# Performance work log

Measured on AMD Instinct MI355X. Metric: run time of the kernel, lower is better.

## Reference

```python
import jax, jax.numpy as jnp
import numpy as np
from jax import lax

NUM_COLS = 4
NUM_ROWS = 4
C = 16          # in_channels
K = 3           # kernel_size
B, H, Wd = 8, 128, 128
W_SCALE = 0.05  # keep activations stable through 16 chained ReLU convs


def setup_inputs() -> dict:
    key = jax.random.key(0)
    k1, k2 = jax.random.split(key, 2)
    x = jax.random.normal(k1, (B, C, H, Wd), dtype=jnp.float32)
    # one conv per grid cell: 3 input slots (left/below-prev/above), 3 output streams (right/up/down)
    W = jax.random.normal(k2, (NUM_COLS, NUM_ROWS, 3 * C, 3 * C, K, K), dtype=jnp.float32) * W_SCALE
    b = jnp.zeros((NUM_COLS, NUM_ROWS, 3 * C), dtype=jnp.float32)
    return {"input_tensor": x, "W": W, "b": b}


def _cell(w, bias, ins):
    # ins: list of 1..3 tensors [B, C, H, W]; zero-pad missing slots to 3*C channels
    if len(ins) < 3:
        pad_shape = (ins[0].shape[0], (3 - len(ins)) * C) + ins[0].shape[2:]
        ins = ins + [jnp.zeros(pad_shape, dtype=ins[0].dtype)]
    x = jnp.concatenate(ins, axis=1)  # [B, 3C, H, W]
    y = lax.conv_general_dilated(
        x, w, window_strides=(1, 1), padding="SAME",
        dimension_numbers=("NCHW", "OIHW", "NCHW"))
    y = jax.nn.relu(y + bias[None, :, None, None])
    right, up, down = jnp.split(y, 3, axis=1)  # each [B, C, H, W]
    return (right, up, down)


def reference(input_tensor, W, b):
    # Wavefront sweep: columns left->right, rows top->bottom.
    # outs[row] holds the (right, up, down) tuple of the most recently computed
    # cell in that row (previous column until overwritten this column).
    outs = [None] * NUM_ROWS
    for col in range(NUM_COLS):
        for row in range(NUM_ROWS):
            if col == 0:
                ins = [input_tensor] if row == 0 else [outs[row - 1][-1]]
            else:
                if row == 0:
                    ins = [outs[row][0], outs[row + 1][1]]
                elif row == NUM_ROWS - 1:
                    ins = [outs[row][0], outs[row - 1][-1]]
                else:
                    ins = [outs[row][0], outs[row + 1][1], outs[row - 1][-1]]
            outs[row] = _cell(W[col, row], b[col, row], ins)
    return outs[-1][0]
```

## Files before the change

### kernel.cpp

```cpp
#include <hip/hip_runtime.h>

#define HW    128
#define PW    130
#define NCELL 16
#define ABUF_PER_CELL 23040
#define ABUF_TOTAL (NCELL * ABUF_PER_CELL)
#define NSTREAMS 15
#define BORDER_PX 516
#define BORDER_TASKS (NSTREAMS * 8 * BORDER_PX * 2)
#define SLOT 5632

typedef _Float16 half8 __attribute__((ext_vector_type(8)));
typedef _Float16 half4 __attribute__((ext_vector_type(4)));
typedef float    f32x4 __attribute__((ext_vector_type(4)));

#define GLD_LDS(gp, lp) __builtin_amdgcn_global_load_lds( \
    (const __attribute__((address_space(1))) void*)(gp),  \
    (__attribute__((address_space(3))) void*)(lp), 16, 0, 0)

__global__ void prep_w_border_k(const float* __restrict__ W,
                                _Float16* __restrict__ Abuf,
                                _Float16* __restrict__ sbase) {
    int idx = blockIdx.x * 256 + threadIdx.x;
    if (idx < ABUF_TOTAL) {
        int j = idx & 7;
        int t = idx >> 3;
        int co = t % 48;   t /= 48;
        int quad = t & 3;  t >>= 2;
        int chunk = t % 5; t /= 5;
        int slot = t % 3;  t /= 3;
        int cell = t;
        int g = chunk * 4 + quad;
        float v = 0.f;
        if (g < 18) {
            int kh = g / 6, r6 = g % 6;
            int kw = r6 >> 1, cg = r6 & 1;
            int ci = slot * 16 + cg * 8 + j;
            v = W[((size_t)(cell * 48 + co) * 48 + ci) * 9 + kh * 3 + kw];
        }
        Abuf[idx] = (_Float16)v;
        return;
    }
    int t = idx - ABUF_TOTAL;
    if (t >= BORDER_TASKS) return;
    int h  = t & 1;
    int pb = t >> 1;
    int p  = pb % BORDER_PX;
    int bb = pb / BORDER_PX;
    int y, x;
    if (p < 260) {
        y = (p < 130) ? 0 : (PW - 1);
        x = p - ((p < 130) ? 0 : 130);
    } else {
        int e = p - 260;
        y = 1 + (e >> 1);
        x = (e & 1) ? (PW - 1) : 0;
    }
    half8 z = {};
    *(half8*)(sbase + (size_t)bb * (PW * PW * 16)
              + ((size_t)y * PW + x) * 16 + h * 8) = z;
}

struct CellIO {
    const _Float16* in0; const _Float16* in1; const _Float16* in2;
    const _Float16* Ac; const float* bc;
    _Float16* o0; _Float16* o1; _Float16* o2;
    float* fout;
};

template<int LIVE, int NIN, bool FIN, bool XIN>
__device__ __forceinline__ void cell_body(const CellIO& P, int b, _Float16* xh,
                                          const float* xsrc)
{
    const int tid = threadIdx.x;
    const int bx = blockIdx.x, by = blockIdx.y;
    const int x0 = bx * 16, y0 = by * 16;
    const int lane = tid & 63, wv = tid >> 6;
    const int n = lane & 15, quad = lane >> 4;
    const int py0 = wv * 4;

    float bv[3][4];
    half8 a0[3][3];

    if constexpr (XIN) {
        for (int task = tid; task < 288; task += 256) {
            int ci = task / 18, iy = task - (task / 18) * 18;
            float v[18];
#pragma unroll
            for (int ix = 0; ix < 18; ++ix) v[ix] = 0.f;
            int gy = y0 + iy - 1;
            if ((unsigned)gy < (unsigned)HW) {
                const float* rp = xsrc + (((size_t)b * 16 + ci) * HW + gy) * HW + x0;
                f32x4 q0 = *(const f32x4*)(rp);
                f32x4 q1 = *(const f32x4*)(rp + 4);
                f32x4 q2 = *(const f32x4*)(rp + 8);
                f32x4 q3 = *(const f32x4*)(rp + 12);
#pragma unroll
                for (int j = 0; j < 4; ++j) {
                    v[1 + j] = q0[j]; v[5 + j] = q1[j];
                    v[9 + j] = q2[j]; v[13 + j] = q3[j];
                }
                if (x0 > 0)       v[0]  = rp[-1];
                if (x0 < HW - 16) v[17] = rp[16];
            }
            int cg = ci >> 3, cj = ci & 7;
#pragma unroll
            for (int ix = 0; ix < 18; ++ix)
                xh[(((iy * 2 + cg) * 18) + ix) * 8 + cj] = (_Float16)v[ix];
        }
        __syncthreads();
    } else {
        const _Float16* const ins[3] = {P.in0, P.in1, P.in2};
        auto stage = [&](int s) {
            const _Float16* src = ins[s] + (size_t)b * (PW * PW * 16)
                                 + ((size_t)(by * 16) * PW + bx * 16) * 16;
            _Float16* base = xh + s * SLOT;
#pragma unroll
            for (int k = 0; k < 3; ++k) {
                int kk = wv + k * 4;
                if (kk < 11) {
                    int u = kk * 64 + lane;
                    int iy = u / 36, r36 = u - iy * 36;
                    int cg = r36 / 18, ix = r36 - cg * 18;
                    GLD_LDS(src + (iy * PW + ix) * 16 + cg * 8, base + kk * 512);
                }
            }
        };
#pragma unroll
        for (int cot = 0; cot < 3; ++cot) {
            if (!(LIVE & (1 << cot))) continue;
#pragma unroll
            for (int r = 0; r < 4; ++r) bv[cot][r] = P.bc[cot * 16 + quad * 4 + r];
        }
        {
            const _Float16* As0 = P.Ac + quad * 384 + n * 8;
#pragma unroll
            for (int c = 0; c < 3; ++c)
#pragma unroll
                for (int cot = 0; cot < 3; ++cot) {
                    if (!(LIVE & (1 << cot))) continue;
                    a0[c][cot] = *(const half8*)(As0 + c * 1536 + cot * 128);
                }
        }
        asm volatile("" ::: "memory");
        stage(0);
        if constexpr (NIN >= 2) {
            asm volatile("" ::: "memory");
#pragma unroll
            for (int s = 1; s < NIN; ++s) stage(s);
            if (wv == 3) asm volatile("s_waitcnt vmcnt(%0)" :: "n"((NIN - 1) * 2) : "memory");
            else         asm volatile("s_waitcnt vmcnt(%0)" :: "n"((NIN - 1) * 3) : "memory");
            __builtin_amdgcn_s_barrier();
            asm volatile("" ::: "memory");
        } else {
            __syncthreads();
        }
    }

    int base_c[5];
#pragma unroll
    for (int c = 0; c < 5; ++c) {
        int g = c * 4 + quad;
        if (g >= 18) g = 0;
        int kh = g / 6, r6 = g % 6;
        int kw = r6 >> 1, cg = r6 & 1;
        base_c[c] = ((py0 + kh) * 2 + cg) * 18 + n + kw;
    }

    constexpr bool PIPE = (!XIN) && (NIN >= 2);
    f32x4 acc[3][4];
#pragma unroll
    for (int cot = 0; cot < 3; ++cot) {
        if (!(LIVE & (1 << cot))) continue;
#pragma unroll
        for (int r = 0; r < 4; ++r) {
            float bvv = XIN ? P.bc[cot * 16 + quad * 4 + r] : bv[cot][r];
#pragma unroll
            for (int nt = 0; nt < 4; ++nt) acc[cot][nt][r] = bvv;
        }
    }

    constexpr int NC = NIN * 5;
#pragma unroll
    for (int i = 0; i < NC; ++i) {
        int s, c;
        if constexpr (PIPE) {
            if (i < 3)                        { s = 0; c = i; }
            else if (i < 3 + 5 * (NIN - 1))   { s = 1 + (i - 3) / 5; c = (i - 3) % 5; }
            else                              { s = 0; c = i - 5 * (NIN - 1); }
        } else { s = i / 5; c = i % 5; }
        if (PIPE && i == 3) __syncthreads();

        const _Float16* sxh = xh + s * SLOT;
        half8 Bh[4];
#pragma unroll
        for (int nt = 0; nt < 4; ++nt)
            Bh[nt] = *(const half8*)(sxh + (base_c[c] + nt * 36) * 8);
        const _Float16* Ab = P.Ac + (size_t)(s * 5 + c) * 1536 + quad * 384 + n * 8;
        half8 ah[3];
#pragma unroll
        for (int cot = 0; cot < 3; ++cot) {
            if (!(LIVE & (1 << cot))) continue;
            if (!XIN && s == 0 && c < 3) ah[cot] = a0[c][cot];
            else                         ah[cot] = *(const half8*)(Ab + cot * 128);
        }
        __builtin_amdgcn_s_setprio(1);
#pragma unroll
        for (int cot = 0; cot < 3; ++cot) {
            if (!(LIVE & (1 << cot))) continue;
#pragma unroll
            for (int nt = 0; nt < 4; ++nt)
                acc[cot][nt] = __builtin_amdgcn_mfma_f32_16x16x32_f16(ah[cot], Bh[nt], acc[cot][nt], 0, 0, 0);
        }
        __builtin_amdgcn_s_setprio(0);
    }

    if constexpr (FIN) {
#pragma unroll
        for (int nt = 0; nt < 4; ++nt) {
            int y = y0 + py0 + nt, xg = x0 + n;
#pragma unroll
            for (int r = 0; r < 4; ++r) {
                float vv = acc[0][nt][r];
                P.fout[(((size_t)b * 16 + quad * 4 + r) * HW + y) * HW + xg] = vv > 0.f ? vv : 0.f;
            }
        }
    } else {
        _Float16* const outs[3] = {P.o0, P.o1, P.o2};
#pragma unroll
        for (int cot = 0; cot < 3; ++cot) {
            if (!(LIVE & (1 << cot))) continue;
            _Float16* op = outs[cot] + (size_t)b * (PW * PW * 16);
#pragma unroll
            for (int nt = 0; nt < 4; ++nt) {
                int y = y0 + py0 + nt;
                half4 hv;
#pragma unroll
                for (int r = 0; r < 4; ++r) {
                    float vv = acc[cot][nt][r];
                    hv[r] = (_Float16)(vv > 0.f ? vv : 0.f);
                }
                *(half4*)(op + ((size_t)(y + 1) * PW + x0 + n + 1) * 16 + quad * 4) = hv;
            }
        }
    }
}

template<int L0, int N0, int L1, int N1, bool FIN, bool XIN>
__global__ __launch_bounds__(256, 4) void cell_k(CellIO P0, CellIO P1,
                                                 const float* xsrc) {
    constexpr int MAXN = (N0 > N1) ? N0 : N1;
    __shared__ __align__(16) _Float16 xh[MAXN * SLOT];
    int b = blockIdx.z & 7;
    if constexpr (L1 > 0) {
        if (blockIdx.z >= 8) { cell_body<L1, N1, false, false>(P1, b, xh, nullptr); return; }
    }
    cell_body<L0, N0, FIN, XIN>(P0, b, xh, xsrc);
}

extern "C" void kernel_launch(void* const* d_in, const int* in_sizes, int n_in,
                              void* d_out, int out_size, void* d_ws, size_t ws_size,
                              hipStream_t stream) {
    const float* x  = (const float*)d_in[0];
    const float* W  = (const float*)d_in[1];
    const float* bi = (const float*)d_in[2];
    float* out = (float*)d_out;

    _Float16* Abuf = (_Float16*)d_ws;
    const size_t abytes = (size_t)NCELL * ABUF_PER_CELL * 2;
    _Float16* q = (_Float16*)((char*)d_ws + abytes);
    _Float16* sbase = q;
    const size_t S = (size_t)8 * PW * PW * 16;

    _Float16 *R[2][4], *U[4], *D[2][2];
    for (int pa = 0; pa < 2; ++pa)
        for (int r = 0; r < 4; ++r) { R[pa][r] = q; q += S; }
    U[0] = nullptr;
    for (int r = 1; r < 4; ++r) { U[r] = q; q += S; }
    D[0][0] = q; q += S; D[0][1] = q; q += S;
    D[1][0] = q; q += S; D[1][1] = q; q += S;

    hipLaunchKernelGGL(prep_w_border_k,
                       dim3((ABUF_TOTAL + BORDER_TASKS + 255) / 256),
                       dim3(256), 0, stream, W, Abuf, sbase);

    auto mkio = [&](int c, int r) -> CellIO {
        CellIO io{};
        if (c == 0) {
            io.in0 = (r == 0) ? nullptr : D[0][(r - 1) & 1];
        } else {
            io.in0 = R[(c - 1) & 1][r];
            if (r == 0)      io.in1 = U[1];
            else if (r == 3) io.in1 = D[c & 1][0];
            else { io.in1 = U[r + 1]; io.in2 = D[c & 1][(r - 1) & 1]; }
        }
        if (c < 3) {
            io.o0 = R[c & 1][r];
            if (r > 0) io.o1 = U[r];
            if (r < 3) io.o2 = D[c & 1][r & 1];
        } else {
            if (r < 3) io.o2 = D[1][r & 1];
            else       io.fout = out;
        }
        io.Ac = Abuf + (size_t)(c * 4 + r) * ABUF_PER_CELL;
        io.bc = bi + (size_t)(c * 4 + r) * 48;
        return io;
    };

    dim3 blk(256), g1(8, 8, 8), g2(8, 8, 16);
#define ONEX(c, r)       do { CellIO a = mkio(c, r); \
    hipLaunchKernelGGL((cell_k<5, 1, 0, 0, false, true>), g1, blk, 0, stream, a, a, x); } while (0)
#define ONE(L, N, c, r)  do { CellIO a = mkio(c, r); \
    hipLaunchKernelGGL((cell_k<L, N, 0, 0, false, false>), g1, blk, 0, stream, a, a, x); } while (0)
#define ONEF(c, r)       do { CellIO a = mkio(c, r); \
    hipLaunchKernelGGL((cell_k<1, 2, 0, 0, true, false>), g1, blk, 0, stream, a, a, x); } while (0)
#define TWO(L0, N0, c0, r0, L1, N1, c1, r1) do { \
    CellIO a = mkio(c0, r0), bb2 = mkio(c1, r1); \
    hipLaunchKernelGGL((cell_k<L0, N0, L1, N1, false, false>), g2, blk, 0, stream, a, bb2, x); } while (0)

    ONEX(0, 0);
    ONE(7, 1, 0, 1);
    TWO(7, 1, 0, 2,  5, 2, 1, 0);
    TWO(3, 1, 0, 3,  7, 3, 1, 1);
    TWO(7, 3, 1, 2,  5, 2, 2, 0);
    TWO(3, 2, 1, 3,  7, 3, 2, 1);
    TWO(7, 3, 2, 2,  4, 2, 3, 0);
    TWO(3, 2, 2, 3,  4, 3, 3, 1);
    ONE(4, 3, 3, 2);
    ONEF(3, 3);
#undef ONEX
#undef ONE
#undef ONEF
#undef TWO
}
```

Baseline: 165.1 us.

## Refine staged-input pipeline with finer vmcnt waits and split B-fragment loads

Shrinks the preloaded slot-0 weight fragments from three chunks to two and restarts the pipelined schedule after two chunks. The single __syncthreads is replaced by per-wave s_waitcnt vmcnt plus s_barrier at chunk boundaries, with a second wait before the third input slot, so later slots can still be in flight while earlier ones are consumed. B fragments are loaded in two halves interleaved with MFMAs to lower register pressure and overlap LDS reads with compute. The manual vmcnt counts depend on the exact number of outstanding global-to-LDS loads per wave, so any mismatch would cause a race.

```diff
diff --git a/kernel.cpp b/kernel.cpp
--- a/kernel.cpp
+++ b/kernel.cpp
@@ -80,7 +80,7 @@
     const int py0 = wv * 4;
 
     float bv[3][4];
-    half8 a0[3][3];
+    half8 a0[2][3];
 
     if constexpr (XIN) {
         for (int task = tid; task < 288; task += 256) {
@@ -135,7 +135,7 @@
         {
             const _Float16* As0 = P.Ac + quad * 384 + n * 8;
 #pragma unroll
-            for (int c = 0; c < 3; ++c)
+            for (int c = 0; c < 2; ++c)
 #pragma unroll
                 for (int cot = 0; cot < 3; ++cot) {
                     if (!(LIVE & (1 << cot))) continue;
@@ -185,34 +185,57 @@
     for (int i = 0; i < NC; ++i) {
         int s, c;
         if constexpr (PIPE) {
-            if (i < 3)                        { s = 0; c = i; }
-            else if (i < 3 + 5 * (NIN - 1))   { s = 1 + (i - 3) / 5; c = (i - 3) % 5; }
+            if (i < 2)                        { s = 0; c = i; }
+            else if (i < 2 + 5 * (NIN - 1))   { s = 1 + (i - 2) / 5; c = (i - 2) % 5; }
             else                              { s = 0; c = i - 5 * (NIN - 1); }
         } else { s = i / 5; c = i % 5; }
-        if (PIPE && i == 3) __syncthreads();
+
+        if constexpr (PIPE) {
+            if (i == 2) {
+                if constexpr (NIN == 3) {
+                    if (wv == 3) asm volatile("s_waitcnt vmcnt(2)" ::: "memory");
+                    else         asm volatile("s_waitcnt vmcnt(3)" ::: "memory");
+                } else {
+                    asm volatile("s_waitcnt vmcnt(0)" ::: "memory");
+                }
+                __builtin_amdgcn_s_barrier();
+                asm volatile("" ::: "memory");
+            }
+            if constexpr (NIN == 3) {
+                if (i == 7) {
+                    asm volatile("s_waitcnt vmcnt(0)" ::: "memory");
+                    __builtin_amdgcn_s_barrier();
+                    asm volatile("" ::: "memory");
+                }
+            }
+        }
 
         const _Float16* sxh = xh + s * SLOT;
-        half8 Bh[4];
-#pragma unroll
-        for (int nt = 0; nt < 4; ++nt)
-            Bh[nt] = *(const half8*)(sxh + (base_c[c] + nt * 36) * 8);
         const _Float16* Ab = P.Ac + (size_t)(s * 5 + c) * 1536 + quad * 384 + n * 8;
         half8 ah[3];
 #pragma unroll
         for (int cot = 0; cot < 3; ++cot) {
             if (!(LIVE & (1 << cot))) continue;
-            if (!XIN && s == 0 && c < 3) ah[cot] = a0[c][cot];
+            if (!XIN && s == 0 && c < 2) ah[cot] = a0[c][cot];
             else                         ah[cot] = *(const half8*)(Ab + cot * 128);
         }
-        __builtin_amdgcn_s_setprio(1);
-#pragma unroll
-        for (int cot = 0; cot < 3; ++cot) {
-            if (!(LIVE & (1 << cot))) continue;
-#pragma unroll
-            for (int nt = 0; nt < 4; ++nt)
-                acc[cot][nt] = __builtin_amdgcn_mfma_f32_16x16x32_f16(ah[cot], Bh[nt], acc[cot][nt], 0, 0, 0);
-        }
-        __builtin_amdgcn_s_setprio(0);
+#pragma unroll
+        for (int np = 0; np < 2; ++np) {
+            half8 Bh[2];
+#pragma unroll
+            for (int t = 0; t < 2; ++t)
+                Bh[t] = *(const half8*)(sxh + (base_c[c] + (np * 2 + t) * 36) * 8);
+            __builtin_amdgcn_s_setprio(1);
+#pragma unroll
+            for (int cot = 0; cot < 3; ++cot) {
+                if (!(LIVE & (1 << cot))) continue;
+#pragma unroll
+                for (int t = 0; t < 2; ++t)
+                    acc[cot][np * 2 + t] = __builtin_amdgcn_mfma_f32_16x16x32_f16(
+                        ah[cot], Bh[t], acc[cot][np * 2 + t], 0, 0, 0);
+            }
+            __builtin_amdgcn_s_setprio(0);
+        }
     }
 
     if constexpr (FIN) {
```

Measured after the change: 169.4 us. +2.6%, slower.

## Fold weight prep and border zeroing into the first cell kernel

Applied to the files above, without the earlier changes.

Removes the separate prep kernel that converted weights to fp16 MFMA layout and zeroed padded borders. The first cell kernel now builds its own cell-0 weights directly into LDS, and its 512 blocks share the remaining weight conversion for cells 1-15 plus the border zeroing. This saves one kernel launch and its serial dependency, at the cost of more LDS and extra work in the first cell kernel, which could lengthen it.

```diff
diff --git a/kernel.cpp b/kernel.cpp
--- a/kernel.cpp
+++ b/kernel.cpp
@@ -9,6 +9,10 @@
 #define BORDER_PX 516
 #define BORDER_TASKS (NSTREAMS * 8 * BORDER_PX * 2)
 #define SLOT 5632
+#define XA_HALFS 7680
+#define PREP_TASKS (15 * ABUF_PER_CELL)
+#define HEAD_TOT (PREP_TASKS + BORDER_TASKS)
+#define HEAD_SPAN ((HEAD_TOT + 511) / 512)
 
 typedef _Float16 half8 __attribute__((ext_vector_type(8)));
 typedef _Float16 half4 __attribute__((ext_vector_type(4)));
@@ -17,49 +21,6 @@
 #define GLD_LDS(gp, lp) __builtin_amdgcn_global_load_lds( \
     (const __attribute__((address_space(1))) void*)(gp),  \
     (__attribute__((address_space(3))) void*)(lp), 16, 0, 0)
-
-__global__ void prep_w_border_k(const float* __restrict__ W,
-                                _Float16* __restrict__ Abuf,
-                                _Float16* __restrict__ sbase) {
-    int idx = blockIdx.x * 256 + threadIdx.x;
-    if (idx < ABUF_TOTAL) {
-        int j = idx & 7;
-        int t = idx >> 3;
-        int co = t % 48;   t /= 48;
-        int quad = t & 3;  t >>= 2;
-        int chunk = t % 5; t /= 5;
-        int slot = t % 3;  t /= 3;
-        int cell = t;
-        int g = chunk * 4 + quad;
-        float v = 0.f;
-        if (g < 18) {
-            int kh = g / 6, r6 = g % 6;
-            int kw = r6 >> 1, cg = r6 & 1;
-            int ci = slot * 16 + cg * 8 + j;
-            v = W[((size_t)(cell * 48 + co) * 48 + ci) * 9 + kh * 3 + kw];
-        }
-        Abuf[idx] = (_Float16)v;
-        return;
-    }
-    int t = idx - ABUF_TOTAL;
-    if (t >= BORDER_TASKS) return;
-    int h  = t & 1;
-    int pb = t >> 1;
-    int p  = pb % BORDER_PX;
-    int bb = pb / BORDER_PX;
-    int y, x;
-    if (p < 260) {
-        y = (p < 130) ? 0 : (PW - 1);
-        x = p - ((p < 130) ? 0 : 130);
-    } else {
-        int e = p - 260;
-        y = 1 + (e >> 1);
-        x = (e & 1) ? (PW - 1) : 0;
-    }
-    half8 z = {};
-    *(half8*)(sbase + (size_t)bb * (PW * PW * 16)
-              + ((size_t)y * PW + x) * 16 + h * 8) = z;
-}
 
 struct CellIO {
     const _Float16* in0; const _Float16* in1; const _Float16* in2;
@@ -70,7 +31,9 @@
 
 template<int LIVE, int NIN, bool FIN, bool XIN>
 __device__ __forceinline__ void cell_body(const CellIO& P, int b, _Float16* xh,
-                                          const float* xsrc)
+                                          _Float16* xa, const float* xsrc,
+                                          const float* Wsrc, _Float16* abufg,
+                                          _Float16* sbaseg)
 {
     const int tid = threadIdx.x;
     const int bx = blockIdx.x, by = blockIdx.y;
@@ -108,6 +71,67 @@
             for (int ix = 0; ix < 18; ++ix)
                 xh[(((iy * 2 + cg) * 18) + ix) * 8 + cj] = (_Float16)v[ix];
         }
+        for (int a = tid; a < XA_HALFS; a += 256) {
+            int j = a & 7;
+            int t = a >> 3;
+            int co = t % 48;  t /= 48;
+            int qd = t & 3;   t >>= 2;
+            int ch = t;
+            int g = ch * 4 + qd;
+            float v = 0.f;
+            if (g < 18) {
+                int kh = g / 6, r6 = g % 6;
+                int kw = r6 >> 1, cg = r6 & 1;
+                int ci = cg * 8 + j;
+                v = Wsrc[((size_t)co * 48 + ci) * 9 + kh * 3 + kw];
+            }
+            xa[a] = (_Float16)v;
+        }
+        {
+            int blin = (blockIdx.z << 6) + (by << 3) + bx;
+            int i0 = blin * HEAD_SPAN;
+            int iend = i0 + HEAD_SPAN;
+            if (iend > HEAD_TOT) iend = HEAD_TOT;
+            for (int idx = i0 + tid; idx < iend; idx += 256) {
+                if (idx < PREP_TASKS) {
+                    int ii = idx + ABUF_PER_CELL;
+                    int j = ii & 7;
+                    int t = ii >> 3;
+                    int co = t % 48;   t /= 48;
+                    int qd = t & 3;    t >>= 2;
+                    int chunk = t % 5; t /= 5;
+                    int slot = t % 3;  t /= 3;
+                    int cell = t;
+                    int g = chunk * 4 + qd;
+                    float v = 0.f;
+                    if (g < 18) {
+                        int kh = g / 6, r6 = g % 6;
+                        int kw = r6 >> 1, cg = r6 & 1;
+                        int ci = slot * 16 + cg * 8 + j;
+                        v = Wsrc[((size_t)(cell * 48 + co) * 48 + ci) * 9 + kh * 3 + kw];
+                    }
+                    abufg[ii] = (_Float16)v;
+                } else {
+                    int t2 = idx - PREP_TASKS;
+                    int h  = t2 & 1;
+                    int pb = t2 >> 1;
+                    int p  = pb % BORDER_PX;
+                    int bb = pb / BORDER_PX;
+                    int y, x;
+                    if (p < 260) {
+                        y = (p < 130) ? 0 : (PW - 1);
+                        x = p - ((p < 130) ? 0 : 130);
+                    } else {
+                        int e = p - 260;
+                        y = 1 + (e >> 1);
+                        x = (e & 1) ? (PW - 1) : 0;
+                    }
+                    half8 z = {};
+                    *(half8*)(sbaseg + (size_t)bb * (PW * PW * 16)
+                              + ((size_t)y * PW + x) * 16 + h * 8) = z;
+                }
+            }
+        }
         __syncthreads();
     } else {
         const _Float16* const ins[3] = {P.in0, P.in1, P.in2};
@@ -196,13 +220,21 @@
 #pragma unroll
         for (int nt = 0; nt < 4; ++nt)
             Bh[nt] = *(const half8*)(sxh + (base_c[c] + nt * 36) * 8);
-        const _Float16* Ab = P.Ac + (size_t)(s * 5 + c) * 1536 + quad * 384 + n * 8;
         half8 ah[3];
-#pragma unroll
-        for (int cot = 0; cot < 3; ++cot) {
-            if (!(LIVE & (1 << cot))) continue;
-            if (!XIN && s == 0 && c < 3) ah[cot] = a0[c][cot];
-            else                         ah[cot] = *(const half8*)(Ab + cot * 128);
+        if constexpr (XIN) {
+#pragma unroll
+            for (int cot = 0; cot < 3; ++cot) {
+                if (!(LIVE & (1 << cot))) continue;
+                ah[cot] = *(const half8*)(xa + c * 1536 + quad * 384 + cot * 128 + n * 8);
+            }
+        } else {
+            const _Float16* Ab = P.Ac + (size_t)(s * 5 + c) * 1536 + quad * 384 + n * 8;
+#pragma unroll
+            for (int cot = 0; cot < 3; ++cot) {
+                if (!(LIVE & (1 << cot))) continue;
+                if (s == 0 && c < 3) ah[cot] = a0[c][cot];
+                else                 ah[cot] = *(const half8*)(Ab + cot * 128);
+            }
         }
         __builtin_amdgcn_s_setprio(1);
 #pragma unroll
@@ -248,14 +280,23 @@
 
 template<int L0, int N0, int L1, int N1, bool FIN, bool XIN>
 __global__ __launch_bounds__(256, 4) void cell_k(CellIO P0, CellIO P1,
-                                                 const float* xsrc) {
+                                                 const float* xsrc,
+                                                 const float* Wsrc,
+                                                 _Float16* abufg,
+                                                 _Float16* sbaseg) {
     constexpr int MAXN = (N0 > N1) ? N0 : N1;
-    __shared__ __align__(16) _Float16 xh[MAXN * SLOT];
+    constexpr int XAH = XIN ? XA_HALFS : 0;
+    __shared__ __align__(16) _Float16 xh[MAXN * SLOT + XAH];
     int b = blockIdx.z & 7;
     if constexpr (L1 > 0) {
-        if (blockIdx.z >= 8) { cell_body<L1, N1, false, false>(P1, b, xh, nullptr); return; }
-    }
-    cell_body<L0, N0, FIN, XIN>(P0, b, xh, xsrc);
+        if (blockIdx.z >= 8) {
+            cell_body<L1, N1, false, false>(P1, b, xh, nullptr, nullptr,
+                                            nullptr, nullptr, nullptr);
+            return;
+        }
+    }
+    cell_body<L0, N0, FIN, XIN>(P0, b, xh, XIN ? (xh + MAXN * SLOT) : nullptr,
+                                xsrc, Wsrc, abufg, sbaseg);
 }
 
 extern "C" void kernel_launch(void* const* d_in, const int* in_sizes, int n_in,
@@ -279,10 +320,6 @@
     for (int r = 1; r < 4; ++r) { U[r] = q; q += S; }
     D[0][0] = q; q += S; D[0][1] = q; q += S;
     D[1][0] = q; q += S; D[1][1] = q; q += S;
-
-    hipLaunchKernelGGL(prep_w_border_k,
-                       dim3((ABUF_TOTAL + BORDER_TASKS + 255) / 256),
-                       dim3(256), 0, stream, W, Abuf, sbase);
 
     auto mkio = [&](int c, int r) -> CellIO {
         CellIO io{};
@@ -309,14 +346,14 @@
 
     dim3 blk(256), g1(8, 8, 8), g2(8, 8, 16);
 #define ONEX(c, r)       do { CellIO a = mkio(c, r); \
-    hipLaunchKernelGGL((cell_k<5, 1, 0, 0, false, true>), g1, blk, 0, stream, a, a, x); } while (0)
+    hipLaunchKernelGGL((cell_k<5, 1, 0, 0, false, true>), g1, blk, 0, stream, a, a, x, W, Abuf, sbase); } while (0)
 #define ONE(L, N, c, r)  do { CellIO a = mkio(c, r); \
-    hipLaunchKernelGGL((cell_k<L, N, 0, 0, false, false>), g1, blk, 0, stream, a, a, x); } while (0)
+    hipLaunchKernelGGL((cell_k<L, N, 0, 0, false, false>), g1, blk, 0, stream, a, a, x, W, Abuf, sbase); } while (0)
 #define ONEF(c, r)       do { CellIO a = mkio(c, r); \
-    hipLaunchKernelGGL((cell_k<1, 2, 0, 0, true, false>), g1, blk, 0, stream, a, a, x); } while (0)
+    hipLaunchKernelGGL((cell_k<1, 2, 0, 0, true, false>), g1, blk, 0, stream, a, a, x, W, Abuf, sbase); } while (0)
 #define TWO(L0, N0, c0, r0, L1, N1, c1, r1) do { \
     CellIO a = mkio(c0, r0), bb2 = mkio(c1, r1); \
-    hipLaunchKernelGGL((cell_k<L0, N0, L1, N1, false, false>), g2, blk, 0, stream, a, bb2, x); } while (0)
+    hipLaunchKernelGGL((cell_k<L0, N0, L1, N1, false, false>), g2, blk, 0, stream, a, bb2, x, W, Abuf, sbase); } while (0)
 
     ONEX(0, 0);
     ONE(7, 1, 0, 1);
```

Measured after the change: 169.9 us. 2.9% more time.

## Read conv input tiles directly from global memory instead of staging in LDS

Applied to the files above, without the earlier changes.

Removes the global_load_lds staging of input halo tiles into shared memory and the barriers that go with it. Each lane now loads its MFMA B operands straight from the padded global activation buffers, relying on L1/L2 caching for reuse across the 3x3 taps. This cuts LDS use and synchronisation, which may allow more resident blocks, but adds redundant global loads and exposes global latency inside the MFMA loop.

```diff
diff --git a/kernel.cpp b/kernel.cpp
--- a/kernel.cpp
+++ b/kernel.cpp
@@ -8,15 +8,10 @@
 #define NSTREAMS 15
 #define BORDER_PX 516
 #define BORDER_TASKS (NSTREAMS * 8 * BORDER_PX * 2)
-#define SLOT 5632
 
 typedef _Float16 half8 __attribute__((ext_vector_type(8)));
 typedef _Float16 half4 __attribute__((ext_vector_type(4)));
 typedef float    f32x4 __attribute__((ext_vector_type(4)));
-
-#define GLD_LDS(gp, lp) __builtin_amdgcn_global_load_lds( \
-    (const __attribute__((address_space(1))) void*)(gp),  \
-    (__attribute__((address_space(3))) void*)(lp), 16, 0, 0)
 
 __global__ void prep_w_border_k(const float* __restrict__ W,
                                 _Float16* __restrict__ Abuf,
@@ -81,6 +76,7 @@
 
     float bv[3][4];
     half8 a0[3][3];
+    const _Float16* srcs[3];
 
     if constexpr (XIN) {
         for (int task = tid; task < 288; task += 256) {
@@ -111,21 +107,10 @@
         __syncthreads();
     } else {
         const _Float16* const ins[3] = {P.in0, P.in1, P.in2};
-        auto stage = [&](int s) {
-            const _Float16* src = ins[s] + (size_t)b * (PW * PW * 16)
-                                 + ((size_t)(by * 16) * PW + bx * 16) * 16;
-            _Float16* base = xh + s * SLOT;
-#pragma unroll
-            for (int k = 0; k < 3; ++k) {
-                int kk = wv + k * 4;
-                if (kk < 11) {
-                    int u = kk * 64 + lane;
-                    int iy = u / 36, r36 = u - iy * 36;
-                    int cg = r36 / 18, ix = r36 - cg * 18;
-                    GLD_LDS(src + (iy * PW + ix) * 16 + cg * 8, base + kk * 512);
-                }
-            }
-        };
+#pragma unroll
+        for (int s = 0; s < NIN; ++s)
+            srcs[s] = ins[s] + (size_t)b * (PW * PW * 16)
+                      + ((size_t)(by * 16) * PW + bx * 16) * 16;
 #pragma unroll
         for (int cot = 0; cot < 3; ++cot) {
             if (!(LIVE & (1 << cot))) continue;
@@ -142,29 +127,17 @@
                     a0[c][cot] = *(const half8*)(As0 + c * 1536 + cot * 128);
                 }
         }
-        asm volatile("" ::: "memory");
-        stage(0);
-        if constexpr (NIN >= 2) {
-            asm volatile("" ::: "memory");
-#pragma unroll
-            for (int s = 1; s < NIN; ++s) stage(s);
-            if (wv == 3) asm volatile("s_waitcnt vmcnt(%0)" :: "n"((NIN - 1) * 2) : "memory");
-            else         asm volatile("s_waitcnt vmcnt(%0)" :: "n"((NIN - 1) * 3) : "memory");
-            __builtin_amdgcn_s_barrier();
-            asm volatile("" ::: "memory");
-        } else {
-            __syncthreads();
-        }
-    }
-
-    int base_c[5];
+    }
+
+    int boff_c[5];
 #pragma unroll
     for (int c = 0; c < 5; ++c) {
         int g = c * 4 + quad;
         if (g >= 18) g = 0;
         int kh = g / 6, r6 = g % 6;
         int kw = r6 >> 1, cg = r6 & 1;
-        base_c[c] = ((py0 + kh) * 2 + cg) * 18 + n + kw;
+        if constexpr (XIN) boff_c[c] = ((py0 + kh) * 2 + cg) * 18 + n + kw;
+        else               boff_c[c] = ((py0 + kh) * PW + n + kw) * 16 + cg * 8;
     }
 
     constexpr bool PIPE = (!XIN) && (NIN >= 2);
@@ -189,13 +162,17 @@
             else if (i < 3 + 5 * (NIN - 1))   { s = 1 + (i - 3) / 5; c = (i - 3) % 5; }
             else                              { s = 0; c = i - 5 * (NIN - 1); }
         } else { s = i / 5; c = i % 5; }
-        if (PIPE && i == 3) __syncthreads();
-
-        const _Float16* sxh = xh + s * SLOT;
+
         half8 Bh[4];
-#pragma unroll
-        for (int nt = 0; nt < 4; ++nt)
-            Bh[nt] = *(const half8*)(sxh + (base_c[c] + nt * 36) * 8);
+        if constexpr (XIN) {
+#pragma unroll
+            for (int nt = 0; nt < 4; ++nt)
+                Bh[nt] = *(const half8*)(xh + (boff_c[c] + nt * 36) * 8);
+        } else {
+#pragma unroll
+            for (int nt = 0; nt < 4; ++nt)
+                Bh[nt] = *(const half8*)(srcs[s] + boff_c[c] + nt * (PW * 16));
+        }
         const _Float16* Ab = P.Ac + (size_t)(s * 5 + c) * 1536 + quad * 384 + n * 8;
         half8 ah[3];
 #pragma unroll
@@ -249,8 +226,8 @@
 template<int L0, int N0, int L1, int N1, bool FIN, bool XIN>
 __global__ __launch_bounds__(256, 4) void cell_k(CellIO P0, CellIO P1,
                                                  const float* xsrc) {
-    constexpr int MAXN = (N0 > N1) ? N0 : N1;
-    __shared__ __align__(16) _Float16 xh[MAXN * SLOT];
+    constexpr int XSH = XIN ? 5184 : 8;
+    __shared__ __align__(16) _Float16 xh[XSH];
     int b = blockIdx.z & 7;
     if constexpr (L1 > 0) {
         if (blockIdx.z >= 8) { cell_body<L1, N1, false, false>(P1, b, xh, nullptr); return; }
```

Measured after the change: 175.8 us. +6.5%, slower.
